# Performance work log

Measured on AMD Instinct MI355X. Metric: run time of the kernel, lower is better.

The kernel has to match this reference:

```python
import jax, jax.numpy as jnp
import numpy as np
import math

B, C, H, W = 2, 256, 64, 64
NUM_HEADS = 8
HEAD_DIM = C // NUM_HEADS
SCALE = math.sqrt(HEAD_DIM)
LN_EPS = 1e-5


def setup_inputs() -> dict:
    key = jax.random.key(0)
    ks = jax.random.split(key, 4)
    std = 1.0 / math.sqrt(C)
    return {
        "x": jax.random.normal(ks[0], (B, C, H, W), dtype=jnp.float32),
        "ln_g": jnp.ones((C,), dtype=jnp.float32),
        "ln_b": jnp.zeros((C,), dtype=jnp.float32),
        "qkv_w": jax.random.normal(ks[1], (3 * C, C), dtype=jnp.float32) * std,
        "qkv_b": jnp.zeros((3 * C,), dtype=jnp.float32),
        "proj_w": jax.random.normal(ks[2], (C, C), dtype=jnp.float32) * std,
        "proj_b": jnp.zeros((C,), dtype=jnp.float32),
    }


def reference(x, ln_g, ln_b, qkv_w, qkv_b, proj_w, proj_b):
    b, c, h, w = x.shape
    n = h * w
    # (B, C, H, W) -> (B, N, C)
    x_flat = x.reshape(b, c, n).transpose(0, 2, 1)
    # LayerNorm over channel dim
    mu = jnp.mean(x_flat, axis=-1, keepdims=True)
    var = jnp.var(x_flat, axis=-1, keepdims=True)
    x_norm = (x_flat - mu) * jax.lax.rsqrt(var + LN_EPS) * ln_g + ln_b
    qkv = x_norm @ qkv_w.T + qkv_b
    qkv = qkv.reshape(b, n, 3, NUM_HEADS, HEAD_DIM).transpose(2, 0, 3, 1, 4)
    q, k, v = qkv[0], qkv[1], qkv[2]
    # Full attention matrix (B, heads, N, N)
    attn = jnp.einsum("bhqd,bhkd->bhqk", q, k) / SCALE
    attn = jax.nn.softmax(attn, axis=-1)
    out = jnp.einsum("bhqk,bhkd->bhqd", attn, v)
    out = out.transpose(0, 2, 1, 3).reshape(b, n, c)
    out = out @ proj_w.T + proj_b
    out = x_flat + out  # residual
    return out.transpose(0, 2, 1).reshape(b, c, h, w)
```

## Files before the change

kernel.cpp:

```cpp
#include <hip/hip_runtime.h>

typedef __bf16 bf16_t;
typedef __bf16 bf16x8 __attribute__((ext_vector_type(8)));
typedef __bf16 bf16x4 __attribute__((ext_vector_type(4)));
typedef float f32x4 __attribute__((ext_vector_type(4)));
typedef float f32x16 __attribute__((ext_vector_type(16)));
typedef unsigned int uint4v __attribute__((ext_vector_type(4)));

#define MFMA16(a, b, c) __builtin_amdgcn_mfma_f32_16x16x32_bf16((a), (b), (c), 0, 0, 0)
#define MFMA32(a, b, c) __builtin_amdgcn_mfma_f32_32x32x16_bf16((a), (b), (c), 0, 0, 0)

static constexpr int N_ = 4096;
static constexpr int TC_ = 768;
static constexpr float QSCALE = 1.4426950408889634f / 5.656854249492380f;

__device__ __forceinline__ unsigned cvtpk(float lo, float hi) {
  unsigned r;
  asm("v_cvt_pk_bf16_f32 %0, %1, %2" : "=v"(r) : "v"(lo), "v"(hi));
  return r;
}
__device__ __forceinline__ float exp2_raw(float x) {
  float r;
  asm("v_exp_f32 %0, %1" : "=v"(r) : "v"(x));
  return r;
}

__global__ __launch_bounds__(256) void conv_w_kernel(
    const float* __restrict__ wq, const float* __restrict__ wp,
    bf16_t* __restrict__ oq, bf16_t* __restrict__ op) {
  int i = blockIdx.x * 256 + threadIdx.x;
  if (i < TC_ * 256) oq[i] = (bf16_t)wq[i];
  if (i < 256 * 256) op[i] = (bf16_t)wp[i];
}

__global__ __launch_bounds__(256) void ln_kernel(
    const float* __restrict__ x, const float* __restrict__ g,
    const float* __restrict__ be, bf16_t* __restrict__ xn) {
  __shared__ float tile[256][33];
  __shared__ float ps1[8][32];
  __shared__ float ps2[8][32];
  __shared__ float smu[32];
  __shared__ float srs[32];
  const int t = (int)threadIdx.x;
  const int b = (int)blockIdx.x >> 7;
  const int n0 = ((int)blockIdx.x & 127) * 32;
  const int nn = t & 31, cq = t >> 5;
#pragma unroll
  for (int c0 = 0; c0 < 256; c0 += 8) {
    int c = c0 + cq;
    tile[c][nn] = x[((size_t)(b * 256 + c)) * N_ + n0 + nn];
  }
  __syncthreads();
  float s1 = 0.f, s2 = 0.f;
#pragma unroll
  for (int i = 0; i < 32; ++i) {
    float v = tile[cq * 32 + i][nn];
    s1 += v;
    s2 += v * v;
  }
  ps1[cq][nn] = s1;
  ps2[cq][nn] = s2;
  __syncthreads();
  if (t < 32) {
    float a1 = 0.f, a2 = 0.f;
#pragma unroll
    for (int p = 0; p < 8; ++p) {
      a1 += ps1[p][t];
      a2 += ps2[p][t];
    }
    float mu = a1 * (1.f / 256.f);
    float var = a2 * (1.f / 256.f) - mu * mu;
    smu[t] = mu;
    srs[t] = rsqrtf(var + 1e-5f);
  }
  __syncthreads();
  const float gc = g[t], bc = be[t];
#pragma unroll 4
  for (int it = 0; it < 32; ++it) {
    float v = (tile[t][it] - smu[it]) * srs[it] * gc + bc;
    xn[((size_t)(b * N_ + n0 + it)) * 256 + t] = (bf16_t)v;
  }
}

__global__ __launch_bounds__(256) void gemm_qkv_kernel(
    const bf16_t* __restrict__ A, const bf16_t* __restrict__ Bw,
    const float* __restrict__ bias, bf16_t* __restrict__ Qf,
    bf16_t* __restrict__ Kf, bf16_t* __restrict__ Vtf) {
  const int tid = (int)threadIdx.x;
  const int w = tid >> 6, l = tid & 63;
  const int l15 = l & 15, lg = l >> 4;
  const int m0 = (int)blockIdx.x * 64 + (w >> 1) * 32;
  const int n0 = (int)blockIdx.y * 64 + (w & 1) * 32;
  f32x4 acc[2][2];
  acc[0][0] = acc[0][1] = acc[1][0] = acc[1][1] = (f32x4){0.f, 0.f, 0.f, 0.f};
  const bf16_t* Ab = A + (size_t)(m0 + l15) * 256 + lg * 8;
  const bf16_t* Bb = Bw + (size_t)(n0 + l15) * 256 + lg * 8;
#pragma unroll
  for (int kk = 0; kk < 256; kk += 32) {
    bf16x8 a0 = *(const bf16x8*)(Ab + kk);
    bf16x8 a1 = *(const bf16x8*)(Ab + 16 * 256 + kk);
    bf16x8 b0 = *(const bf16x8*)(Bb + kk);
    bf16x8 b1 = *(const bf16x8*)(Bb + 16 * 256 + kk);
    acc[0][0] = MFMA16(a0, b0, acc[0][0]);
    acc[0][1] = MFMA16(a0, b1, acc[0][1]);
    acc[1][0] = MFMA16(a1, b0, acc[1][0]);
    acc[1][1] = MFMA16(a1, b1, acc[1][1]);
  }
  const int part = (int)blockIdx.y >> 2;
#pragma unroll
  for (int mi = 0; mi < 2; ++mi)
#pragma unroll
    for (int ji = 0; ji < 2; ++ji) {
      const int n = n0 + ji * 16 + l15;
      const int h = (n >> 5) & 7, d = n & 31;
      const float bn = bias[n];
#pragma unroll
      for (int r = 0; r < 4; ++r) {
        const int m = m0 + mi * 16 + lg * 4 + r;
        const int b = m >> 12, token = m & 4095;
        float v = acc[mi][ji][r] + bn;
        const int ht = ((b * 8 + h) * 128 + (token >> 5)) * 2;
        if (part == 0) {
          v *= QSCALE;
          size_t idx = ((size_t)(ht + (d >> 4)) * 64 + ((d >> 3) & 1) * 32 + (token & 31)) * 8 + (d & 7);
          Qf[idx] = (bf16_t)v;
        } else if (part == 1) {
          size_t idx = ((size_t)(ht + (d >> 4)) * 64 + ((d >> 3) & 1) * 32 + (token & 31)) * 8 + (d & 7);
          Kf[idx] = (bf16_t)v;
        } else {
          const int kv5 = token & 31;
          size_t idx = ((size_t)(ht + (kv5 >> 4)) * 64 + ((kv5 >> 2) & 1) * 32 + d) * 8
                       + (kv5 & 3) + ((kv5 >> 3) & 1) * 4;
          Vtf[idx] = (bf16_t)v;
        }
      }
    }
}

__global__ __launch_bounds__(512, 4) void flash2_kernel(
    const bf16_t* __restrict__ Qf, const bf16_t* __restrict__ Kf,
    const bf16_t* __restrict__ Vtf, bf16_t* __restrict__ aout) {
  __shared__ float lds_o[4][16][64];
  __shared__ float lds_l[4][64];
  int bid = (int)blockIdx.x;
  bid = (bid & 7) * 64 + (bid >> 3);
  const int head = bid >> 5;
  const int qtg = bid & 31;
  const int w = (int)threadIdx.x >> 6, l = (int)threadIdx.x & 63;
  const int half = w >> 2, wq = w & 3;
  const int qt = qtg * 4 + wq;

  const bf16_t* qp = Qf + (size_t)head * 131072 + (size_t)qt * 1024 + l * 8;
  const bf16x8 qf0 = *(const bf16x8*)qp;
  const bf16x8 qf1 = *(const bf16x8*)(qp + 512);
  const bf16_t* kp = Kf + (size_t)head * 131072 + (size_t)half * 65536 + l * 8;
  const bf16_t* vp = Vtf + (size_t)head * 131072 + (size_t)half * 65536 + l * 8;

  bf16x8 ones;
#pragma unroll
  for (int i = 0; i < 8; ++i) ones[i] = (bf16_t)1.0f;

  f32x16 o = {};
  f32x16 lacc = {};

  bf16x8 vf0 = *(const bf16x8*)vp;
  bf16x8 vf1 = *(const bf16x8*)(vp + 512);
  bf16x8 g0 = *(const bf16x8*)(kp + 1024);
  bf16x8 g1 = *(const bf16x8*)(kp + 1536);
  bf16x8 g2 = *(const bf16x8*)(vp + 1024);
  bf16x8 g3 = *(const bf16x8*)(vp + 1536);
  f32x16 s_cur = {};
  {
    bf16x8 k00 = *(const bf16x8*)kp;
    bf16x8 k01 = *(const bf16x8*)(kp + 512);
    s_cur = MFMA32(k00, qf0, s_cur);
    s_cur = MFMA32(k01, qf1, s_cur);
  }

#pragma unroll 2
  for (int t = 0; t < 64; ++t) {
    const bf16_t* kn = kp + (size_t)(t + 2) * 1024;
    const bf16_t* vn = vp + (size_t)(t + 2) * 1024;
    bf16x8 h0 = *(const bf16x8*)kn;
    bf16x8 h1 = *(const bf16x8*)(kn + 512);
    bf16x8 h2 = *(const bf16x8*)vn;
    bf16x8 h3 = *(const bf16x8*)(vn + 512);

    f32x16 s_next = {};
    s_next = MFMA32(g0, qf0, s_next);
    s_next = MFMA32(g1, qf1, s_next);

    float p[16];
#pragma unroll
    for (int r = 0; r < 16; ++r) p[r] = exp2_raw(s_cur[r]);

    uint4v u0 = {cvtpk(p[0], p[1]), cvtpk(p[2], p[3]), cvtpk(p[4], p[5]), cvtpk(p[6], p[7])};
    uint4v u1 = {cvtpk(p[8], p[9]), cvtpk(p[10], p[11]), cvtpk(p[12], p[13]), cvtpk(p[14], p[15])};
    bf16x8 pf0 = __builtin_bit_cast(bf16x8, u0);
    bf16x8 pf1 = __builtin_bit_cast(bf16x8, u1);

    o = MFMA32(vf0, pf0, o);
    o = MFMA32(vf1, pf1, o);
    lacc = MFMA32(ones, pf0, lacc);
    lacc = MFMA32(ones, pf1, lacc);

    s_cur = s_next;
    vf0 = g2; vf1 = g3;
    g0 = h0; g1 = h1; g2 = h2; g3 = h3;
  }

  if (half == 1) {
#pragma unroll
    for (int r = 0; r < 16; ++r) lds_o[wq][r][l] = o[r];
    lds_l[wq][l] = lacc[0];
  }
  __syncthreads();
  if (half == 0) {
    float l_tot = lacc[0] + lds_l[wq][l];
#pragma unroll
    for (int r = 0; r < 16; ++r) o[r] += lds_o[wq][r][l];
    const float inv = 1.0f / l_tot;
    const int q = l & 31, hi = l >> 5;
    const int row = (head >> 3) * N_ + qt * 32 + q;
    bf16_t* ob = aout + (size_t)row * 256 + (head & 7) * 32;
#pragma unroll
    for (int g = 0; g < 4; ++g) {
      bf16x4 st;
#pragma unroll
      for (int j = 0; j < 4; ++j) st[j] = (bf16_t)(o[g * 4 + j] * inv);
      *(bf16x4*)(ob + hi * 4 + g * 8) = st;
    }
  }
}

__global__ __launch_bounds__(256) void gemm_proj_kernel(
    const bf16_t* __restrict__ A, const bf16_t* __restrict__ Bw,
    const float* __restrict__ bias, const float* __restrict__ x,
    float* __restrict__ outp) {
  const int tid = (int)threadIdx.x;
  const int w = tid >> 6, l = tid & 63;
  const int l15 = l & 15, lg = l >> 4;
  const int m0 = (int)blockIdx.x * 64 + (w >> 1) * 32;
  const int n0 = (int)blockIdx.y * 64 + (w & 1) * 32;
  f32x4 acc[2][2];
  acc[0][0] = acc[0][1] = acc[1][0] = acc[1][1] = (f32x4){0.f, 0.f, 0.f, 0.f};
  const bf16_t* Ab = A + (size_t)(m0 + l15) * 256 + lg * 8;
  const bf16_t* Bb = Bw + (size_t)(n0 + l15) * 256 + lg * 8;
#pragma unroll
  for (int kk = 0; kk < 256; kk += 32) {
    bf16x8 a0 = *(const bf16x8*)(Ab + kk);
    bf16x8 a1 = *(const bf16x8*)(Ab + 16 * 256 + kk);
    bf16x8 b0 = *(const bf16x8*)(Bb + kk);
    bf16x8 b1 = *(const bf16x8*)(Bb + 16 * 256 + kk);
    acc[0][0] = MFMA16(a0, b0, acc[0][0]);
    acc[0][1] = MFMA16(a0, b1, acc[0][1]);
    acc[1][0] = MFMA16(a1, b0, acc[1][0]);
    acc[1][1] = MFMA16(a1, b1, acc[1][1]);
  }
#pragma unroll
  for (int mi = 0; mi < 2; ++mi)
#pragma unroll
    for (int ji = 0; ji < 2; ++ji) {
      int n = n0 + ji * 16 + l15;
      int mb = m0 + mi * 16 + lg * 4;
      int bb = mb >> 12;
      int nn = mb & 4095;
      size_t oidx = ((size_t)(bb * 256 + n)) * N_ + nn;
      float bn = bias[n];
      float4 xr = *(const float4*)(x + oidx);
      float4 res;
      res.x = xr.x + acc[mi][ji][0] + bn;
      res.y = xr.y + acc[mi][ji][1] + bn;
      res.z = xr.z + acc[mi][ji][2] + bn;
      res.w = xr.w + acc[mi][ji][3] + bn;
      *(float4*)(outp + oidx) = res;
    }
}

extern "C" void kernel_launch(void* const* d_in, const int* in_sizes, int n_in,
                              void* d_out, int out_size, void* d_ws, size_t ws_size,
                              hipStream_t stream) {
  (void)in_sizes; (void)n_in; (void)out_size; (void)ws_size;
  const float* x = (const float*)d_in[0];
  const float* ln_g = (const float*)d_in[1];
  const float* ln_b = (const float*)d_in[2];
  const float* qkv_w = (const float*)d_in[3];
  const float* qkv_b = (const float*)d_in[4];
  const float* proj_w = (const float*)d_in[5];
  const float* proj_b = (const float*)d_in[6];
  float* out = (float*)d_out;

  char* wsp = (char*)d_ws;
  bf16_t* xn = (bf16_t*)(wsp);
  bf16_t* wq = (bf16_t*)(wsp + 4194304);
  bf16_t* wp = (bf16_t*)(wsp + 4587520);
  bf16_t* Qf = (bf16_t*)(wsp + 4718592);
  bf16_t* Kf = (bf16_t*)(wsp + 8912896);
  bf16_t* Vtf = (bf16_t*)(wsp + 13107200);
  bf16_t* aout = (bf16_t*)(wsp + 17301504);

  hipLaunchKernelGGL(conv_w_kernel, dim3(768), dim3(256), 0, stream, qkv_w, proj_w, wq, wp);
  hipLaunchKernelGGL(ln_kernel, dim3(256), dim3(256), 0, stream, x, ln_g, ln_b, xn);
  hipLaunchKernelGGL(gemm_qkv_kernel, dim3(128, 12), dim3(256), 0, stream, xn, wq, qkv_b, Qf, Kf, Vtf);
  hipLaunchKernelGGL(flash2_kernel, dim3(512), dim3(512), 0, stream, Qf, Kf, Vtf, aout);
  hipLaunchKernelGGL(gemm_proj_kernel, dim3(128, 4), dim3(256), 0, stream, aout, wp, proj_b, x, out);
}
```

Baseline: 105.1 us.

## Merge LN and weight-convert kernels; software-pipeline PV MFMAs behind exp

Weight bf16 conversion and LayerNorm now run in one launch, with blocks past 256 doing the weight conversion, which removes one kernel launch. In the attention loop the P·V and row-sum MFMAs for the previous tile are issued before the exp of the current scores, so matrix work can overlap the transcendental ALU work. The prefetch index is clamped to 63 to avoid reading past the K/V buffers. The cost is extra registers for the previous P and V fragments and a drain step after the loop.

Result: faster. 99.42 us (-5.4%).

```diff
diff --git a/kernel.cpp b/kernel.cpp
--- a/kernel.cpp
+++ b/kernel.cpp
@@ -25,25 +25,26 @@
   return r;
 }
 
-__global__ __launch_bounds__(256) void conv_w_kernel(
-    const float* __restrict__ wq, const float* __restrict__ wp,
+__global__ __launch_bounds__(256) void prep_kernel(
+    const float* __restrict__ x, const float* __restrict__ g,
+    const float* __restrict__ be, bf16_t* __restrict__ xn,
+    const float* __restrict__ wqf, const float* __restrict__ wpf,
     bf16_t* __restrict__ oq, bf16_t* __restrict__ op) {
-  int i = blockIdx.x * 256 + threadIdx.x;
-  if (i < TC_ * 256) oq[i] = (bf16_t)wq[i];
-  if (i < 256 * 256) op[i] = (bf16_t)wp[i];
-}
-
-__global__ __launch_bounds__(256) void ln_kernel(
-    const float* __restrict__ x, const float* __restrict__ g,
-    const float* __restrict__ be, bf16_t* __restrict__ xn) {
+  const int t = (int)threadIdx.x;
+  const int bid = (int)blockIdx.x;
+  if (bid >= 256) {
+    int i = (bid - 256) * 256 + t;
+    if (i < TC_ * 256) oq[i] = (bf16_t)wqf[i];
+    if (i < 256 * 256) op[i] = (bf16_t)wpf[i];
+    return;
+  }
   __shared__ float tile[256][33];
   __shared__ float ps1[8][32];
   __shared__ float ps2[8][32];
   __shared__ float smu[32];
   __shared__ float srs[32];
-  const int t = (int)threadIdx.x;
-  const int b = (int)blockIdx.x >> 7;
-  const int n0 = ((int)blockIdx.x & 127) * 32;
+  const int b = bid >> 7;
+  const int n0 = (bid & 127) * 32;
   const int nn = t & 31, cq = t >> 5;
 #pragma unroll
   for (int c0 = 0; c0 < 256; c0 += 8) {
@@ -163,6 +164,10 @@
   f32x16 o = {};
   f32x16 lacc = {};
 
+  bf16x8 pf0_prev = {};
+  bf16x8 pf1_prev = {};
+  bf16x8 vfp0 = {};
+  bf16x8 vfp1 = {};
   bf16x8 vf0 = *(const bf16x8*)vp;
   bf16x8 vf1 = *(const bf16x8*)(vp + 512);
   bf16x8 g0 = *(const bf16x8*)(kp + 1024);
@@ -179,8 +184,9 @@
 
 #pragma unroll 2
   for (int t = 0; t < 64; ++t) {
-    const bf16_t* kn = kp + (size_t)(t + 2) * 1024;
-    const bf16_t* vn = vp + (size_t)(t + 2) * 1024;
+    const int tn = (t + 2 < 63) ? (t + 2) : 63;
+    const bf16_t* kn = kp + (size_t)tn * 1024;
+    const bf16_t* vn = vp + (size_t)tn * 1024;
     bf16x8 h0 = *(const bf16x8*)kn;
     bf16x8 h1 = *(const bf16x8*)(kn + 512);
     bf16x8 h2 = *(const bf16x8*)vn;
@@ -190,24 +196,28 @@
     s_next = MFMA32(g0, qf0, s_next);
     s_next = MFMA32(g1, qf1, s_next);
 
+    o = MFMA32(vfp0, pf0_prev, o);
+    o = MFMA32(vfp1, pf1_prev, o);
+    lacc = MFMA32(ones, pf0_prev, lacc);
+    lacc = MFMA32(ones, pf1_prev, lacc);
+
     float p[16];
 #pragma unroll
     for (int r = 0; r < 16; ++r) p[r] = exp2_raw(s_cur[r]);
-
     uint4v u0 = {cvtpk(p[0], p[1]), cvtpk(p[2], p[3]), cvtpk(p[4], p[5]), cvtpk(p[6], p[7])};
     uint4v u1 = {cvtpk(p[8], p[9]), cvtpk(p[10], p[11]), cvtpk(p[12], p[13]), cvtpk(p[14], p[15])};
-    bf16x8 pf0 = __builtin_bit_cast(bf16x8, u0);
-    bf16x8 pf1 = __builtin_bit_cast(bf16x8, u1);
-
-    o = MFMA32(vf0, pf0, o);
-    o = MFMA32(vf1, pf1, o);
-    lacc = MFMA32(ones, pf0, lacc);
-    lacc = MFMA32(ones, pf1, lacc);
-
+
+    pf0_prev = __builtin_bit_cast(bf16x8, u0);
+    pf1_prev = __builtin_bit_cast(bf16x8, u1);
+    vfp0 = vf0; vfp1 = vf1;
     s_cur = s_next;
     vf0 = g2; vf1 = g3;
     g0 = h0; g1 = h1; g2 = h2; g3 = h3;
   }
+  o = MFMA32(vfp0, pf0_prev, o);
+  o = MFMA32(vfp1, pf1_prev, o);
+  lacc = MFMA32(ones, pf0_prev, lacc);
+  lacc = MFMA32(ones, pf1_prev, lacc);
 
   if (half == 1) {
 #pragma unroll
@@ -299,8 +309,8 @@
   bf16_t* Vtf = (bf16_t*)(wsp + 13107200);
   bf16_t* aout = (bf16_t*)(wsp + 17301504);
 
-  hipLaunchKernelGGL(conv_w_kernel, dim3(768), dim3(256), 0, stream, qkv_w, proj_w, wq, wp);
-  hipLaunchKernelGGL(ln_kernel, dim3(256), dim3(256), 0, stream, x, ln_g, ln_b, xn);
+  hipLaunchKernelGGL(prep_kernel, dim3(1024), dim3(256), 0, stream,
+                     x, ln_g, ln_b, xn, qkv_w, proj_w, wq, wp);
   hipLaunchKernelGGL(gemm_qkv_kernel, dim3(128, 12), dim3(256), 0, stream, xn, wq, qkv_b, Qf, Kf, Vtf);
   hipLaunchKernelGGL(flash2_kernel, dim3(512), dim3(512), 0, stream, Qf, Kf, Vtf, aout);
   hipLaunchKernelGGL(gemm_proj_kernel, dim3(128, 4), dim3(256), 0, stream, aout, wp, proj_b, x, out);
```
